# Kernel tuning notes

Measured on AMD Instinct MI355X. Metric: run time of the kernel, lower is better.

## Reference

```python
import jax, jax.numpy as jnp
import numpy as np

NX, NTEST, DX, DY = 8192, 8192, 32, 32
VAR_EPS = 0.01   # params['var_eps']
L_MEAN = 8.0     # fit kernel lengthscale after l_scale adjustment
L_VAR = 8.0


def _rbf(X, Y, l):
    # pairwise squared distances: [Nx, Nq]
    d2 = (jnp.sum(X * X, axis=1)[:, None]
          + jnp.sum(Y * Y, axis=1)[None, :]
          - 2.0 * (X @ Y.T))
    return jnp.exp(-jnp.maximum(d2, 0.0) / (2.0 * l * l))


def setup_inputs() -> dict:
    key = jax.random.key(0)
    ks = jax.random.split(key, 10)
    inp = {
        'x_mu':   jax.random.normal(ks[0], (NTEST, DX), jnp.float32),
        'y_eta':  jax.random.normal(ks[1], (NTEST, DY), jnp.float32),
        'y_mean': jax.random.normal(ks[2], (NTEST, DY), jnp.float32),
        'y_var':  jax.random.normal(ks[3], (NTEST, DY), jnp.float32) * 0.1,
        'X_mean': jax.random.normal(ks[4], (NX, DX + DY), jnp.float32),
        'X_var':  jax.random.normal(ks[5], (NX, DX + 2 * DY), jnp.float32),
        'Z_mean': jax.random.normal(ks[6], (NX, DY), jnp.float32),
        'Z_var':  jax.random.normal(ks[7], (NX, DY), jnp.float32),
        # precomputed inverse Gram matrices (stand-ins with same compute pattern)
        'kXXmean_inv': jax.random.normal(ks[8], (NX, NX), jnp.float32) * 0.001,
        'kXXvar_inv':  jax.random.normal(ks[9], (NX, NX), jnp.float32) * 0.001,
    }
    return inp


def reference(x_mu, y_eta, y_mean, y_var, X_mean, X_var, Z_mean, Z_var,
              kXXmean_inv, kXXvar_inv):
    # map_mean: x_mean = [x_mu, y_mean + y_var]
    x_mean = jnp.concatenate([x_mu, y_mean + y_var], axis=1)          # [Nq, DX+DY]
    Lambda_mean = kXXmean_inv @ Z_mean                                # [Nx, DY]
    z_mean = _rbf(X_mean, x_mean, L_MEAN).T @ Lambda_mean             # [Nq, DY]

    # map_var: x_var = [x_mu, var_eps * flip(y_eta), y_mean + y_var]
    x_var = jnp.concatenate(
        [x_mu, VAR_EPS * jnp.flip(y_eta, axis=0), y_mean + y_var], axis=1)
    Lambda_var = kXXvar_inv @ Z_var                                   # [Nx, DY]
    z_var = _rbf(X_var, x_var, L_VAR).T @ Lambda_var                  # [Nq, DY]

    # transported sample: (y_mean + z_mean) + (y_var + z_var)
    return (y_mean + z_mean) + (y_var + z_var)
```

## Files before the change

kernel.cpp:

```cpp
#include <hip/hip_runtime.h>
#include <stdint.h>

#define NXR 8192
#define NQR 8192
#define DMEAN 64
#define DVAR 96
#define DYC 32

typedef float f32x4 __attribute__((ext_vector_type(4)));
typedef __bf16 bf16x8 __attribute__((ext_vector_type(8)));
typedef unsigned short us4v __attribute__((ext_vector_type(4)));

__device__ __forceinline__ unsigned short f2bf(float f) {
    union { float f; uint32_t u; } v; v.f = f;
    uint32_t r = (v.u + 0x7FFFu + ((v.u >> 16) & 1u)) >> 16;
    return (unsigned short)r;
}
__device__ __forceinline__ float bf2f(unsigned short b) {
    union { uint32_t u; float f; } v; v.u = ((uint32_t)b) << 16;
    return v.f;
}
__device__ __forceinline__ int perm_idx(int k, int c) {
    return (k >> 5) * 1024 + (c >> 4) * 512 +
           ((((k >> 3) & 3) * 16 + (c & 15)) * 8) + (k & 7);
}

typedef const __attribute__((address_space(1))) uint32_t* as1_u32p;
typedef __attribute__((address_space(3))) uint32_t* as3_u32p;
__device__ __forceinline__ void gl_lds16(const void* g, void* l) {
    __builtin_amdgcn_global_load_lds((as1_u32p)g, (as3_u32p)l, 16, 0, 0);
}

__global__ __launch_bounds__(256) void k_prep(
    const float* __restrict__ x_mu, const float* __restrict__ y_eta,
    const float* __restrict__ y_mean, const float* __restrict__ y_var,
    const float* __restrict__ X_mean, const float* __restrict__ X_var,
    const float* __restrict__ Z_mean, const float* __restrict__ Z_var,
    unsigned short* __restrict__ Qm, unsigned short* __restrict__ Qv,
    unsigned short* __restrict__ Xm, unsigned short* __restrict__ Xv,
    unsigned short* __restrict__ Zpm, unsigned short* __restrict__ Zpv,
    float* __restrict__ qn_m, float* __restrict__ qn_v,
    float* __restrict__ Xn_m, float* __restrict__ Xn_v,
    float* __restrict__ out)
{
    int w = threadIdx.x >> 6;
    int lane = threadIdx.x & 63;
    int row = blockIdx.x * 4 + w;

    float accq_m = 0.f, accq_v = 0.f;
    if (lane < 32) {
        int c = lane;
        float xm = x_mu[row * 32 + c];
        float s  = y_mean[row * 32 + c] + y_var[row * 32 + c];
        float e  = 0.01f * y_eta[(NQR - 1 - row) * 32 + c];
        unsigned short bx = f2bf(xm), bs = f2bf(s), be = f2bf(e);
        Qm[row * DMEAN + c] = bx;  Qm[row * DMEAN + 32 + c] = bs;
        Qv[row * DVAR + c] = bx;   Qv[row * DVAR + 32 + c] = be;
        Qv[row * DVAR + 64 + c] = bs;
        out[row * 32 + c] = s;
        Zpm[perm_idx(row, c)] = f2bf(Z_mean[row * 32 + c]);
        Zpv[perm_idx(row, c)] = f2bf(Z_var[row * 32 + c]);
        float fx = bf2f(bx), fs = bf2f(bs), fe = bf2f(be);
        accq_m = fx * fx + fs * fs;
        accq_v = fx * fx + fe * fe + fs * fs;
    }
    float a = X_mean[row * DMEAN + lane];
    unsigned short ba = f2bf(a);
    Xm[row * DMEAN + lane] = ba;
    float fa = bf2f(ba);
    float accx_m = fa * fa;

    float b0 = X_var[row * DVAR + lane];
    unsigned short bb0 = f2bf(b0);
    Xv[row * DVAR + lane] = bb0;
    float fb0 = bf2f(bb0);
    float accx_v = fb0 * fb0;
    if (lane < 32) {
        float b1 = X_var[row * DVAR + 64 + lane];
        unsigned short bb1 = f2bf(b1);
        Xv[row * DVAR + 64 + lane] = bb1;
        float fb1 = bf2f(bb1);
        accx_v += fb1 * fb1;
    }
    for (int o = 32; o >= 1; o >>= 1) {
        accq_m += __shfl_xor(accq_m, o, 64);
        accq_v += __shfl_xor(accq_v, o, 64);
        accx_m += __shfl_xor(accx_m, o, 64);
        accx_v += __shfl_xor(accx_v, o, 64);
    }
    if (lane == 0) {
        qn_m[row] = accq_m; qn_v[row] = accq_v;
        Xn_m[row] = accx_m; Xn_v[row] = accx_v;
    }
}

__global__ __launch_bounds__(256, 4) void k_lambda(
    const float* __restrict__ kXXm, const float* __restrict__ kXXv,
    const unsigned short* __restrict__ Zpm, const unsigned short* __restrict__ Zpv,
    unsigned short* __restrict__ Lpm, unsigned short* __restrict__ Lpv)
{
    __shared__ __align__(16) char smem[32768];
    int b = blockIdx.x;
    int mat = b & 1;
    int rg = b >> 1;
    const float* A = mat ? kXXv : kXXm;
    const unsigned short* Zp = mat ? Zpv : Zpm;
    unsigned short* Lp = mat ? Lpv : Lpm;

    int w = threadIdx.x >> 6, lane = threadIdx.x & 63;
    int r0 = rg * 16;
    char* wb = smem + w * 8192;

    int rtA  = lane >> 3;
    int srcA = ((lane & 7) * 16) ^ (rtA << 4);
    const char* A0 = (const char*)A + ((size_t)(r0 + rtA) * NXR) * 4
                     + (size_t)w * 8192 + srcA;
    const char* A1 = A0 + (size_t)8 * NXR * 4;
    const char* Zb = (const char*)Zp + (size_t)w * 64 * 2048 + lane * 16;

    int rt = lane & 15, g = lane >> 4;
    int ro0 = rt * 128 + (((g * 32) + 0)  ^ ((rt & 7) << 4));
    int ro1 = rt * 128 + (((g * 32) + 16) ^ ((rt & 7) << 4));

    f32x4 acc0 = {0.f, 0.f, 0.f, 0.f}, acc1 = {0.f, 0.f, 0.f, 0.f};

    auto stage = [&](int t) {
        char* base = wb + (t & 1) * 4096;
        size_t ko = (size_t)t * 128;
        gl_lds16(A0 + ko, base);
        gl_lds16(A1 + ko, base + 1024);
        gl_lds16(Zb + (size_t)t * 2048, base + 2048);
        gl_lds16(Zb + (size_t)t * 2048 + 1024, base + 3072);
    };
    auto process = [&](int t) {
        char* base = wb + (t & 1) * 4096;
        f32x4 a0 = *(const f32x4*)(base + ro0);
        f32x4 a1 = *(const f32x4*)(base + ro1);
        bf16x8 bz0 = *(const bf16x8*)(base + 2048 + lane * 16);
        bf16x8 bz1 = *(const bf16x8*)(base + 3072 + lane * 16);
        union { unsigned short u[8]; bf16x8 v; } af;
#pragma unroll
        for (int j = 0; j < 4; ++j) { af.u[j] = f2bf(a0[j]); af.u[4 + j] = f2bf(a1[j]); }
        acc0 = __builtin_amdgcn_mfma_f32_16x16x32_bf16(af.v, bz0, acc0, 0, 0, 0);
        acc1 = __builtin_amdgcn_mfma_f32_16x16x32_bf16(af.v, bz1, acc1, 0, 0, 0);
    };

    stage(0);
#pragma unroll 1
    for (int t = 0; t < 63; ++t) {
        stage(t + 1);
        asm volatile("s_waitcnt vmcnt(4)" ::: "memory");
        process(t);
    }
    asm volatile("s_waitcnt vmcnt(0)" ::: "memory");
    process(63);

    __syncthreads();
    float (*red)[64][8] = (float (*)[64][8])smem;
    *(f32x4*)&red[w][lane][0] = acc0;
    *(f32x4*)&red[w][lane][4] = acc1;
    __syncthreads();
    int tix = threadIdx.x;
    int row = tix >> 4, c16 = tix & 15;
    int ls = (row >> 2) * 16 + c16;
    int rr = row & 3;
    float v0 = red[0][ls][rr] + red[1][ls][rr] + red[2][ls][rr] + red[3][ls][rr];
    float v1 = red[0][ls][4 + rr] + red[1][ls][4 + rr] +
               red[2][ls][4 + rr] + red[3][ls][4 + rr];
    Lp[perm_idx(r0 + row, c16)]      = f2bf(v0);
    Lp[perm_idx(r0 + row, c16 + 16)] = f2bf(v1);
}

__global__ __launch_bounds__(256) void k_transport(
    const unsigned short* __restrict__ Qm, const unsigned short* __restrict__ Qv,
    const unsigned short* __restrict__ Xm, const unsigned short* __restrict__ Xv,
    const float* __restrict__ qn_m, const float* __restrict__ qn_v,
    const float* __restrict__ Xn_m, const float* __restrict__ Xn_v,
    const unsigned short* __restrict__ Lpm, const unsigned short* __restrict__ Lpv,
    float* __restrict__ out)
{
    __shared__ unsigned short KT[4][16 * 40];
    int b = blockIdx.x;
    int mat = b & 1;
    int split = (b >> 1) & 3;
    int qb = b >> 3;
    const unsigned short* Q = mat ? Qv : Qm;
    const unsigned short* X = mat ? Xv : Xm;
    const float* qn = mat ? qn_v : qn_m;
    const float* Xn = mat ? Xn_v : Xn_m;
    const unsigned short* Lp = mat ? Lpv : Lpm;
    const int D = mat ? DVAR : DMEAN;
    const int nk0 = mat ? 3 : 2;

    int w = threadIdx.x >> 6, lane = threadIdx.x & 63;
    int q0 = qb * 64 + w * 16;
    int qrow = q0 + (lane & 15);
    int g = lane >> 4;

    bf16x8 Qf[3];
    for (int c0 = 0; c0 < nk0; ++c0)
        Qf[c0] = *(const bf16x8*)(Q + (size_t)qrow * D + c0 * 32 + g * 8);
    float qn_c = qn[qrow];
    unsigned short* lds = KT[w];

    f32x4 z0 = {0.f, 0.f, 0.f, 0.f}, z1 = {0.f, 0.f, 0.f, 0.f};
    for (int xb = 0; xb < 64; ++xb) {
        int x0 = split * 2048 + xb * 32;
#pragma unroll
        for (int sub = 0; sub < 2; ++sub) {
            int xrow = x0 + sub * 16 + (lane & 15);
            const unsigned short* Xr = X + (size_t)xrow * D + g * 8;
            f32x4 s = {0.f, 0.f, 0.f, 0.f};
            s = __builtin_amdgcn_mfma_f32_16x16x32_bf16(*(const bf16x8*)(Xr), Qf[0], s, 0, 0, 0);
            s = __builtin_amdgcn_mfma_f32_16x16x32_bf16(*(const bf16x8*)(Xr + 32), Qf[1], s, 0, 0, 0);
            if (nk0 == 3)
                s = __builtin_amdgcn_mfma_f32_16x16x32_bf16(*(const bf16x8*)(Xr + 64), Qf[2], s, 0, 0, 0);
            int xnb = x0 + sub * 16 + g * 4;
            f32x4 xn4 = *(const f32x4*)(Xn + xnb);
            us4v kv;
#pragma unroll
            for (int r = 0; r < 4; ++r) {
                float d2 = xn4[r] + qn_c - 2.0f * s[r];
                d2 = fmaxf(d2, 0.0f);
                kv[r] = f2bf(__expf(-d2 * 0.0078125f));
            }
            *(us4v*)(lds + (lane & 15) * 40 + sub * 16 + g * 4) = kv;
        }
        asm volatile("s_waitcnt lgkmcnt(0)" ::: "memory");
        bf16x8 Kf = *(const bf16x8*)(lds + (lane & 15) * 40 + g * 8);
        const unsigned short* lpb = Lp + (size_t)(x0 >> 5) * 1024 + lane * 8;
        bf16x8 l0 = *(const bf16x8*)(lpb);
        bf16x8 l1 = *(const bf16x8*)(lpb + 512);
        z0 = __builtin_amdgcn_mfma_f32_16x16x32_bf16(Kf, l0, z0, 0, 0, 0);
        z1 = __builtin_amdgcn_mfma_f32_16x16x32_bf16(Kf, l1, z1, 0, 0, 0);
    }
    int rbase = q0 + g * 4;
    int c0 = lane & 15;
#pragma unroll
    for (int r = 0; r < 4; ++r) {
        atomicAdd(&out[(rbase + r) * 32 + c0], z0[r]);
        atomicAdd(&out[(rbase + r) * 32 + c0 + 16], z1[r]);
    }
}

extern "C" void kernel_launch(void* const* d_in, const int* in_sizes, int n_in,
                              void* d_out, int out_size, void* d_ws, size_t ws_size,
                              hipStream_t stream) {
    const float* x_mu   = (const float*)d_in[0];
    const float* y_eta  = (const float*)d_in[1];
    const float* y_mean = (const float*)d_in[2];
    const float* y_var  = (const float*)d_in[3];
    const float* X_mean = (const float*)d_in[4];
    const float* X_var  = (const float*)d_in[5];
    const float* Z_mean = (const float*)d_in[6];
    const float* Z_var  = (const float*)d_in[7];
    const float* kXXm   = (const float*)d_in[8];
    const float* kXXv   = (const float*)d_in[9];
    float* out = (float*)d_out;

    char* ws = (char*)d_ws;
    size_t off = 0;
    auto carve = [&](size_t bytes) { char* p = ws + off; off += (bytes + 255) & ~(size_t)255; return p; };
    unsigned short* Qm  = (unsigned short*)carve(NQR * DMEAN * 2);
    unsigned short* Qv  = (unsigned short*)carve(NQR * DVAR * 2);
    unsigned short* Xm  = (unsigned short*)carve(NXR * DMEAN * 2);
    unsigned short* Xv  = (unsigned short*)carve(NXR * DVAR * 2);
    unsigned short* Zpm = (unsigned short*)carve(NXR * DYC * 2);
    unsigned short* Zpv = (unsigned short*)carve(NXR * DYC * 2);
    unsigned short* Lpm = (unsigned short*)carve(NXR * DYC * 2);
    unsigned short* Lpv = (unsigned short*)carve(NXR * DYC * 2);
    float* qn_m = (float*)carve(NQR * 4);
    float* qn_v = (float*)carve(NQR * 4);
    float* Xn_m = (float*)carve(NXR * 4);
    float* Xn_v = (float*)carve(NXR * 4);

    k_prep<<<dim3(2048), dim3(256), 0, stream>>>(
        x_mu, y_eta, y_mean, y_var, X_mean, X_var, Z_mean, Z_var,
        Qm, Qv, Xm, Xv, Zpm, Zpv, qn_m, qn_v, Xn_m, Xn_v, out);
    k_lambda<<<dim3(1024), dim3(256), 0, stream>>>(kXXm, kXXv, Zpm, Zpv, Lpm, Lpv);
    k_transport<<<dim3(1024), dim3(256), 0, stream>>>(
        Qm, Qv, Xm, Xv, qn_m, qn_v, Xn_m, Xn_v, Lpm, Lpv, out);
}
```

Before: 711.7 us.

## Deepen k_lambda pipeline with larger stages and register-held Z tiles

Restructures the Lambda matvec kernel so each pipeline stage loads 4x more K (512 bytes per row) of the fp32 inverse Gram matrix into LDS. The Z tiles now go straight into registers via global loads instead of through LDS. Loop trip count drops from 64 to 16 with two-slot double buffering and more outstanding memory ops, aimed at better hiding HBM latency on this bandwidth-bound 2x256MB read. LDS doubles to 64KB and occupancy hint drops to 2 blocks per CU, which may reduce latency hiding from wave parallelism.

```diff
diff --git a/kernel.cpp b/kernel.cpp
--- a/kernel.cpp
+++ b/kernel.cpp
@@ -94,12 +94,12 @@
     }
 }
 
-__global__ __launch_bounds__(256, 4) void k_lambda(
+__global__ __launch_bounds__(256, 2) void k_lambda(
     const float* __restrict__ kXXm, const float* __restrict__ kXXv,
     const unsigned short* __restrict__ Zpm, const unsigned short* __restrict__ Zpv,
     unsigned short* __restrict__ Lpm, unsigned short* __restrict__ Lpv)
 {
-    __shared__ __align__(16) char smem[32768];
+    __shared__ __align__(16) char smem[65536];
     int b = blockIdx.x;
     int mat = b & 1;
     int rg = b >> 1;
@@ -109,51 +109,69 @@
 
     int w = threadIdx.x >> 6, lane = threadIdx.x & 63;
     int r0 = rg * 16;
-    char* wb = smem + w * 8192;
-
-    int rtA  = lane >> 3;
-    int srcA = ((lane & 7) * 16) ^ (rtA << 4);
-    const char* A0 = (const char*)A + ((size_t)(r0 + rtA) * NXR) * 4
-                     + (size_t)w * 8192 + srcA;
-    const char* A1 = A0 + (size_t)8 * NXR * 4;
-    const char* Zb = (const char*)Zp + (size_t)w * 64 * 2048 + lane * 16;
+    char* wlds = smem + w * 16384;
+
+    int hl = lane >> 5;
+    int cb = (lane & 31) * 16;
+    const char* Ag = (const char*)A + (size_t)(r0 + hl) * 32768 + w * 8192;
+    const char* Zq = (const char*)Zp + (size_t)w * 131072 + lane * 16;
 
     int rt = lane & 15, g = lane >> 4;
-    int ro0 = rt * 128 + (((g * 32) + 0)  ^ ((rt & 7) << 4));
-    int ro1 = rt * 128 + (((g * 32) + 16) ^ ((rt & 7) << 4));
+    int sw = (rt & 7) << 4;
+    int rd0 = w * 16384 + rt * 512 + ((g * 32) ^ sw);
+    int rd1 = rd0 ^ 16;
 
     f32x4 acc0 = {0.f, 0.f, 0.f, 0.f}, acc1 = {0.f, 0.f, 0.f, 0.f};
-
-    auto stage = [&](int t) {
-        char* base = wb + (t & 1) * 4096;
-        size_t ko = (size_t)t * 128;
-        gl_lds16(A0 + ko, base);
-        gl_lds16(A1 + ko, base + 1024);
-        gl_lds16(Zb + (size_t)t * 2048, base + 2048);
-        gl_lds16(Zb + (size_t)t * 2048 + 1024, base + 3072);
+    bf16x8 zA[8], zB[8];
+
+    auto stageA = [&](int t, int slot) {
+        char* d = wlds + slot;
+        const char* s = Ag + (size_t)t * 512;
+#pragma unroll
+        for (int i = 0; i < 8; ++i) {
+            int sw_i = ((2 * i + hl) & 7) << 4;
+            gl_lds16(s + (size_t)i * 65536 + (cb ^ sw_i), d + i * 1024);
+        }
     };
-    auto process = [&](int t) {
-        char* base = wb + (t & 1) * 4096;
-        f32x4 a0 = *(const f32x4*)(base + ro0);
-        f32x4 a1 = *(const f32x4*)(base + ro1);
-        bf16x8 bz0 = *(const bf16x8*)(base + 2048 + lane * 16);
-        bf16x8 bz1 = *(const bf16x8*)(base + 3072 + lane * 16);
-        union { unsigned short u[8]; bf16x8 v; } af;
-#pragma unroll
-        for (int j = 0; j < 4; ++j) { af.u[j] = f2bf(a0[j]); af.u[4 + j] = f2bf(a1[j]); }
-        acc0 = __builtin_amdgcn_mfma_f32_16x16x32_bf16(af.v, bz0, acc0, 0, 0, 0);
-        acc1 = __builtin_amdgcn_mfma_f32_16x16x32_bf16(af.v, bz1, acc1, 0, 0, 0);
+    auto loadZ = [&](bf16x8* z, int t) {
+        const char* zb = Zq + (size_t)t * 8192;
+#pragma unroll
+        for (int kk = 0; kk < 4; ++kk) {
+            z[2 * kk]     = *(const bf16x8*)(zb + kk * 2048);
+            z[2 * kk + 1] = *(const bf16x8*)(zb + kk * 2048 + 1024);
+        }
     };
-
-    stage(0);
+    auto procST = [&](int slot, const bf16x8* z) {
+#pragma unroll
+        for (int kk = 0; kk < 4; ++kk) {
+            f32x4 a0 = *(const f32x4*)(smem + rd0 + slot + kk * 128);
+            f32x4 a1 = *(const f32x4*)(smem + rd1 + slot + kk * 128);
+            union { unsigned short u[8]; bf16x8 v; } af;
+#pragma unroll
+            for (int j = 0; j < 4; ++j) { af.u[j] = f2bf(a0[j]); af.u[4 + j] = f2bf(a1[j]); }
+            acc0 = __builtin_amdgcn_mfma_f32_16x16x32_bf16(af.v, z[2 * kk], acc0, 0, 0, 0);
+            acc1 = __builtin_amdgcn_mfma_f32_16x16x32_bf16(af.v, z[2 * kk + 1], acc1, 0, 0, 0);
+        }
+    };
+
+    stageA(0, 0);    loadZ(zA, 0);
+    stageA(1, 8192); loadZ(zB, 1);
 #pragma unroll 1
-    for (int t = 0; t < 63; ++t) {
-        stage(t + 1);
-        asm volatile("s_waitcnt vmcnt(4)" ::: "memory");
-        process(t);
-    }
+    for (int tt = 0; tt < 7; ++tt) {
+        int t = 2 * tt;
+        asm volatile("s_waitcnt vmcnt(16)" ::: "memory");
+        procST(0, zA);
+        asm volatile("" ::: "memory");
+        stageA(t + 2, 0);   loadZ(zA, t + 2);
+        asm volatile("s_waitcnt vmcnt(16)" ::: "memory");
+        procST(8192, zB);
+        asm volatile("" ::: "memory");
+        stageA(t + 3, 8192); loadZ(zB, t + 3);
+    }
+    asm volatile("s_waitcnt vmcnt(16)" ::: "memory");
+    procST(0, zA);
     asm volatile("s_waitcnt vmcnt(0)" ::: "memory");
-    process(63);
+    procST(8192, zB);
 
     __syncthreads();
     float (*red)[64][8] = (float (*)[64][8])smem;
```

Result: faster. 687.4 us (-3.4%).
